# Kernel tuning notes

Hardware: AMD Instinct MI355X
Metric: run time of the kernel (lower is better)

Reference implementation:

```python
import jax, jax.numpy as jnp
import numpy as np

N_NODES = 50000
N_EDGES = 400000
N_E2E = 1600000
F_N = 128
F_E = 64
H = 128
NEG_SLOPE = 0.2


def setup_inputs() -> dict:
    key = jax.random.key(0)
    ks = jax.random.split(key, 8)
    x_node = jax.random.normal(ks[0], (N_NODES, F_N), dtype=jnp.float32)
    edge_attr = jax.random.normal(ks[1], (N_EDGES, F_E), dtype=jnp.float32)
    edge_index = jax.random.randint(ks[2], (2, N_EDGES), 0, N_NODES, dtype=jnp.int64)
    edge_edge_index = jax.random.randint(ks[3], (2, N_E2E), 0, N_EDGES, dtype=jnp.int64)
    # xavier-uniform-like init scales
    def xavier(k, shape):
        fan_in, fan_out = shape[1], shape[0]
        lim = jnp.sqrt(6.0 / (fan_in + fan_out)).astype(jnp.float32)
        return jax.random.uniform(k, shape, jnp.float32, -lim, lim)
    Wn = xavier(ks[4], (H, F_N))          # lin_node.weight
    We = xavier(ks[5], (H, F_E))          # lin_edge.weight
    an = xavier(ks[6], (1, 2 * H))[0]     # att_n.weight, flattened to [2H]
    ae = xavier(ks[7], (1, 2 * H))[0]     # att_e.weight, flattened to [2H]
    return {"x_node": x_node, "edge_attr": edge_attr, "edge_index": edge_index,
            "edge_edge_index": edge_edge_index, "Wn": Wn, "We": We, "an": an, "ae": ae}


def _segment_softmax(score, seg, num_segments):
    m = jax.ops.segment_max(score, seg, num_segments=num_segments)
    ex = jnp.exp(score - m[seg])
    denom = jax.ops.segment_sum(ex, seg, num_segments=num_segments)
    return ex / denom[seg]


def reference(x_node, edge_attr, edge_index, edge_edge_index, Wn, We, an, ae):
    E = edge_attr.shape[0]
    h = x_node @ Wn.T      # [N, H]
    g = edge_attr @ We.T   # [E, H]

    # ---- node-based neighbors of each edge (its 2 endpoints) ----
    u, v = edge_index[0], edge_index[1]
    e_rep = jnp.concatenate([jnp.arange(E), jnp.arange(E)])   # segment ids [2E]
    n_for_e = jnp.concatenate([u, v])                          # [2E]
    a1, a2 = an[:H], an[H:]   # split cat([g, h]) @ an into two dots
    h_nbr = h[n_for_e]                                         # [2E, H]
    score_ne = jax.nn.leaky_relu(g[e_rep] @ a1 + h_nbr @ a2, NEG_SLOPE)
    alpha_ne = _segment_softmax(score_ne, e_rep, E)
    s_n = jax.ops.segment_sum(alpha_ne[:, None] * h_nbr, e_rep, num_segments=E)
    cnt_n = jax.ops.segment_sum(jnp.ones_like(alpha_ne), e_rep, num_segments=E)
    e_from_nodes = jax.nn.relu(s_n / jnp.maximum(cnt_n, 1.0)[:, None])

    # ---- edge-based neighbors (edges sharing a node) ----
    e_src, e_nbr = edge_edge_index[0], edge_edge_index[1]
    b1, b2 = ae[:H], ae[H:]
    g_nbr = g[e_nbr]                                           # [E2E, H]
    score_ee = jax.nn.leaky_relu(g[e_src] @ b1 + g_nbr @ b2, NEG_SLOPE)
    alpha_ee = _segment_softmax(score_ee, e_src, E)
    s_e = jax.ops.segment_sum(alpha_ee[:, None] * g_nbr, e_src, num_segments=E)
    cnt_e = jax.ops.segment_sum(jnp.ones_like(alpha_ee), e_src, num_segments=E)
    e_from_edges = jax.nn.relu(s_e / jnp.maximum(cnt_e, 1.0)[:, None])

    return jnp.concatenate([e_from_nodes, e_from_edges], axis=-1)  # [E, 2H]
```

## Files before the change

kernel.cpp:

```cpp
#include <hip/hip_runtime.h>
#include <hip/hip_bf16.h>

#define N_NODES 50000
#define N_EDGES 400000
#define N_E2E   1600000
#define F_N 128
#define F_E 64
#define H   128
#define NEG_SLOPE 0.2f
#define CAP 24

typedef __hip_bfloat16 bf16;
typedef __attribute__((ext_vector_type(8))) short bf16x8;
typedef __attribute__((ext_vector_type(4))) float f32x4;


__device__ inline float2 upk(unsigned int v) {
    union { unsigned int u; float f; } a, b;
    a.u = v << 16;
    b.u = v & 0xffff0000u;
    return make_float2(a.f, b.f);
}
__device__ inline unsigned int f2bfbits(float f) {
    union { float f; unsigned int u; } a; a.f = f;
    return (a.u + 0x7fffu + ((a.u >> 16) & 1u)) >> 16;
}
__device__ inline float lrelu(float x) { return x > 0.f ? x : NEG_SLOPE * x; }

__device__ inline float ldf(const void* p, size_t i, int isf32) {
    return isf32 ? ((const float*)p)[i] : __bfloat162float(((const bf16*)p)[i]);
}
__device__ inline int ldidx(const int* p, long long k, int is64) {
    return is64 ? p[2 * k] : p[k];
}

__device__ inline void loadA4(const void* p, int isf32, size_t idx, float* v) {
    if (isf32) {
        const float4 f = *(const float4*)((const float*)p + idx);
        v[0] = f.x; v[1] = f.y; v[2] = f.z; v[3] = f.w;
    } else {
        const uint2 u = *(const uint2*)((const bf16*)p + idx);
        float2 a = upk(u.x), b = upk(u.y);
        v[0] = a.x; v[1] = a.y; v[2] = b.x; v[3] = b.y;
    }
}
__device__ inline void stash(unsigned short* s, unsigned off, unsigned loOff, const float* v) {
    unsigned hb[4], lb[4];
    #pragma unroll
    for (int j = 0; j < 4; ++j) {
        unsigned hbits = f2bfbits(v[j]);
        union { unsigned u; float f; } hf; hf.u = hbits << 16;
        hb[j] = hbits;
        lb[j] = f2bfbits(v[j] - hf.f);
    }
    *(uint2*)((char*)s + off)         = make_uint2(hb[0] | (hb[1] << 16), hb[2] | (hb[3] << 16));
    *(uint2*)((char*)s + loOff + off) = make_uint2(lb[0] | (lb[1] << 16), lb[2] | (lb[3] << 16));
}

__global__ __launch_bounds__(256) void k_pat(unsigned int* __restrict__ o,
                                             long long n, unsigned int pat) {
    long long i = (long long)blockIdx.x * 256 + threadIdx.x;
    long long stride = (long long)gridDim.x * 256;
    for (; i < n; i += stride) o[i] = pat;
}

__global__ __launch_bounds__(256) void k_init(const unsigned int* x, const unsigned int* ea,
                                              const unsigned int* Wn, const unsigned int* We,
                                              const unsigned int* an, const unsigned int* ae,
                                              const unsigned int* ei, const unsigned int* eei,
                                              int* __restrict__ flags, int* __restrict__ cnt) {
    int i = blockIdx.x * 256 + threadIdx.x;
    if (i < N_EDGES) cnt[i] = 0;
    if (blockIdx.x == 0) {
        int t = threadIdx.x;
        if (t < 6) {
            const unsigned int* p = t == 0 ? x : t == 1 ? ea : t == 2 ? Wn
                                  : t == 3 ? We : t == 4 ? an : ae;
            int inrange = 0;
            for (int k = 0; k < 64; k++) {
                unsigned int e = (p[k] >> 7) & 0xFFu;
                if (e >= 100u && e <= 140u) inrange++;
            }
            flags[t] = (inrange < 48) ? 1 : 0;
        } else if (t < 8) {
            const unsigned int* p = (t == 6) ? ei : eei;
            int allzero = 1;
            for (int k = 1; k < 128; k += 2) if (p[k] != 0u) allzero = 0;
            flags[t] = allzero;
        }
    }
}

template<int K>
__global__ __launch_bounds__(256) void k_gemm(const void* __restrict__ A,
                                              const void* __restrict__ W,
                                              const int* __restrict__ flags,
                                              int faIdx, int fwIdx, int M,
                                              bf16* __restrict__ out,
                                              const void* __restrict__ an,
                                              const void* __restrict__ ae,
                                              float* __restrict__ dot0,
                                              float* __restrict__ dot1,
                                              float* __restrict__ dot2) {
    __shared__ unsigned short sA[2 * 128 * 64];
    __shared__ unsigned short sB[2 * 128 * 64];
    constexpr unsigned ALO = 128u * 64u * 2u;
    constexpr unsigned BLO = 128u * 64u * 2u;
    const int t = threadIdx.x;
    const int e0 = blockIdx.x * 128;
    const int fa = flags[faIdx], fw = flags[fwIdx];
    const int w = t >> 6, l = t & 63;
    const int lr = l & 15, lk = l >> 4;
    const unsigned sxor = (unsigned)((l & 7) << 4);

    f32x4 acc[8][2];
    #pragma unroll
    for (int mt = 0; mt < 8; ++mt)
        #pragma unroll
        for (int nt = 0; nt < 2; ++nt)
            acc[mt][nt] = (f32x4){0.f, 0.f, 0.f, 0.f};

    #pragma unroll
    for (int kt = 0; kt < K / 64; ++kt) {
        if (kt) __syncthreads();
        #pragma unroll
        for (int c0 = 0; c0 < 2048; c0 += 256) {
            int c = c0 + t;
            int r = c >> 4, kc = (c & 15) << 2;
            float v[4];
            int e = e0 + r;
            if (e < M) loadA4(A, fa, (size_t)e * K + kt * 64 + kc, v);
            else { v[0] = v[1] = v[2] = v[3] = 0.f; }
            stash(sA, (unsigned)((r * 64 + kc) * 2) ^ ((unsigned)(r & 7) << 4), ALO, v);
        }
        #pragma unroll
        for (int c0 = 0; c0 < 2048; c0 += 256) {
            int c = c0 + t;
            int r = c >> 4, kc = (c & 15) << 2;
            float v[4];
            loadA4(W, fw, (size_t)r * K + kt * 64 + kc, v);
            stash(sB, (unsigned)((r * 64 + kc) * 2) ^ ((unsigned)(r & 7) << 4), BLO, v);
        }
        __syncthreads();
        const char* pA = (const char*)sA;
        const char* pB = (const char*)sB;
        #pragma unroll
        for (int ks = 0; ks < 2; ++ks) {
            const unsigned ko = (unsigned)((ks * 32 + lk * 8) * 2);
            bf16x8 bh[2], bl[2];
            #pragma unroll
            for (int nt = 0; nt < 2; ++nt) {
                unsigned off = ((unsigned)((w * 32 + nt * 16 + lr) * 128) + ko) ^ sxor;
                bh[nt] = *(const bf16x8*)(pB + off);
                bl[nt] = *(const bf16x8*)(pB + BLO + off);
            }
            #pragma unroll
            for (int mt = 0; mt < 8; ++mt) {
                unsigned off = ((unsigned)((mt * 16 + lr) * 128) + ko) ^ sxor;
                bf16x8 ah = *(const bf16x8*)(pA + off);
                bf16x8 al = *(const bf16x8*)(pA + ALO + off);
                #pragma unroll
                for (int nt = 0; nt < 2; ++nt) {
                    acc[mt][nt] = __builtin_amdgcn_mfma_f32_16x16x32_bf16(ah, bh[nt], acc[mt][nt], 0, 0, 0);
                    acc[mt][nt] = __builtin_amdgcn_mfma_f32_16x16x32_bf16(ah, bl[nt], acc[mt][nt], 0, 0, 0);
                    acc[mt][nt] = __builtin_amdgcn_mfma_f32_16x16x32_bf16(al, bh[nt], acc[mt][nt], 0, 0, 0);
                }
            }
        }
    }
    #pragma unroll
    for (int mt = 0; mt < 8; ++mt)
        #pragma unroll
        for (int i = 0; i < 4; ++i) {
            int e = e0 + mt * 16 + lk * 4 + i;
            if (e < M) {
                #pragma unroll
                for (int nt = 0; nt < 2; ++nt)
                    out[(size_t)e * 128 + (w * 32 + nt * 16 + lr)] =
                        __float2bfloat16(acc[mt][nt][i]);
            }
        }
    __syncthreads();
    float* sd = (float*)sA;
    const int fan = flags[4], fae = flags[5];
    const int c0i = w * 32 + lr, c1i = c0i + 16;
    constexpr int ND = (K == 64) ? 3 : 1;
    float av[ND][2];
    if constexpr (K == 64) {
        av[0][0] = ldf(an, c0i, fan);      av[0][1] = ldf(an, c1i, fan);
        av[1][0] = ldf(ae, c0i, fae);      av[1][1] = ldf(ae, c1i, fae);
        av[2][0] = ldf(ae, H + c0i, fae);  av[2][1] = ldf(ae, H + c1i, fae);
    } else {
        av[0][0] = ldf(an, H + c0i, fan);  av[0][1] = ldf(an, H + c1i, fan);
    }
    #pragma unroll
    for (int d = 0; d < ND; ++d)
        #pragma unroll
        for (int mt = 0; mt < 8; ++mt)
            #pragma unroll
            for (int i = 0; i < 4; ++i) {
                float p = acc[mt][0][i] * av[d][0] + acc[mt][1][i] * av[d][1];
                #pragma unroll
                for (int off = 1; off < 16; off <<= 1) p += __shfl_xor(p, off, 64);
                if (lr == 0) sd[(d * 4 + w) * 128 + mt * 16 + lk * 4 + i] = p;
            }
    __syncthreads();
    for (int idx = t; idx < 128 * ND; idx += 256) {
        int d = idx >> 7, row = idx & 127;
        float vs = sd[(d * 4 + 0) * 128 + row] + sd[(d * 4 + 1) * 128 + row]
                 + sd[(d * 4 + 2) * 128 + row] + sd[(d * 4 + 3) * 128 + row];
        int e = e0 + row;
        if (e < M) (d == 0 ? dot0 : d == 1 ? dot1 : dot2)[e] = vs;
    }
}

__global__ __launch_bounds__(256) void k_node(const int* __restrict__ ei,
                                              const int* __restrict__ flags,
                                              const bf16* __restrict__ h,
                                              const float* __restrict__ ha2,
                                              const float* __restrict__ ga1,
                                              void* __restrict__ out) {
    int e = blockIdx.x * 8 + (threadIdx.x >> 5);
    int lane = threadIdx.x & 31;
    int is64 = flags[6], fo = flags[0];
    int u = ldidx(ei, e, is64);
    int v = ldidx(ei, (long long)N_EDGES + e, is64);
    float ga = ga1[e];
    float su = lrelu(ga + ha2[u]);
    float sv = lrelu(ga + ha2[v]);
    float m = fmaxf(su, sv);
    float eu = __expf(su - m), ev = __expf(sv - m);
    float inv = 1.f / (eu + ev);
    float wu = (eu * inv) * 0.5f;
    float wv = (ev * inv) * 0.5f;
    const uint2* hw = (const uint2*)h;
    uint2 qu = hw[(size_t)u * 32 + lane];
    uint2 qv = hw[(size_t)v * 32 + lane];
    float2 u0 = upk(qu.x), u1 = upk(qu.y);
    float2 v0 = upk(qv.x), v1 = upk(qv.y);
    float c0 = wu * u0.x + wv * v0.x;
    float c1 = wu * u0.y + wv * v0.y;
    float c2 = wu * u1.x + wv * v1.x;
    float c3 = wu * u1.y + wv * v1.y;
    float r0 = c0 > 0.f ? c0 : 0.f; if (c0 != c0) r0 = c0;
    float r1 = c1 > 0.f ? c1 : 0.f; if (c1 != c1) r1 = c1;
    float r2 = c2 > 0.f ? c2 : 0.f; if (c2 != c2) r2 = c2;
    float r3 = c3 > 0.f ? c3 : 0.f; if (c3 != c3) r3 = c3;
    if (fo) {
        float4* o = (float4*)((float*)out + (size_t)e * 256 + 4 * lane);
        *o = make_float4(r0, r1, r2, r3);
    } else {
        uint2 pk;
        pk.x = f2bfbits(r0) | (f2bfbits(r1) << 16);
        pk.y = f2bfbits(r2) | (f2bfbits(r3) << 16);
        ((uint2*)((bf16*)out + (size_t)e * 256))[lane] = pk;
    }
}

__global__ __launch_bounds__(256) void k_fill(const int* __restrict__ eei,
                                              const int* __restrict__ flags,
                                              int* __restrict__ cnt,
                                              int* __restrict__ bucket) {
    int k = blockIdx.x * 256 + threadIdx.x;
    if (k >= N_E2E) return;
    int is64 = flags[7];
    int src = ldidx(eei, k, is64);
    int nbr = ldidx(eei, (long long)N_E2E + k, is64);
    int j = atomicAdd(&cnt[src], 1);
    if (j < CAP) bucket[(size_t)src * CAP + j] = nbr;
}

__global__ __launch_bounds__(256) void k_ee(const int* __restrict__ cnt,
                                            const int* __restrict__ bucket,
                                            const float* __restrict__ gb1,
                                            const float* __restrict__ gb2,
                                            const bf16* __restrict__ g,
                                            const int* __restrict__ flags,
                                            void* __restrict__ out) {
    int e = blockIdx.x * 8 + (threadIdx.x >> 5);
    int lane = threadIdx.x & 31;
    int base = threadIdx.x & 32;
    int fo = flags[0];
    int c = cnt[e]; if (c > CAP) c = CAP;
    float s = -1e30f; int mynbr = 0;
    if (lane < c) {
        mynbr = bucket[(size_t)e * CAP + lane];
        s = lrelu(gb1[e] + gb2[mynbr]);
    }
    float m = s;
    #pragma unroll
    for (int off = 16; off; off >>= 1) m = fmaxf(m, __shfl_xor(m, off, 64));
    float ex = (lane < c) ? __expf(s - m) : 0.f;
    float denom = ex;
    #pragma unroll
    for (int off = 16; off; off >>= 1) denom += __shfl_xor(denom, off, 64);
    float invd = denom > 0.f ? 1.f / denom : 0.f;
    float ax = 0.f, ay = 0.f, az = 0.f, aw = 0.f;
    const uint2* __restrict__ gw = (const uint2*)g;
    for (int j0 = 0; j0 < c; j0 += 4) {
        float a0 = __shfl(ex, base + j0, 64) * invd;
        float a1 = __shfl(ex, base + j0 + 1, 64) * invd;
        float a2 = __shfl(ex, base + j0 + 2, 64) * invd;
        float a3 = __shfl(ex, base + j0 + 3, 64) * invd;
        int n0 = __shfl(mynbr, base + j0, 64);
        int n1 = __shfl(mynbr, base + j0 + 1, 64);
        int n2 = __shfl(mynbr, base + j0 + 2, 64);
        int n3 = __shfl(mynbr, base + j0 + 3, 64);
        uint2 q0 = gw[(size_t)n0 * 32 + lane];
        uint2 q1 = gw[(size_t)n1 * 32 + lane];
        uint2 q2 = gw[(size_t)n2 * 32 + lane];
        uint2 q3 = gw[(size_t)n3 * 32 + lane];
        float2 l0 = upk(q0.x), h0 = upk(q0.y);
        float2 l1 = upk(q1.x), h1 = upk(q1.y);
        float2 l2 = upk(q2.x), h2 = upk(q2.y);
        float2 l3 = upk(q3.x), h3 = upk(q3.y);
        ax += a0 * l0.x; ay += a0 * l0.y; az += a0 * h0.x; aw += a0 * h0.y;
        ax += a1 * l1.x; ay += a1 * l1.y; az += a1 * h1.x; aw += a1 * h1.y;
        ax += a2 * l2.x; ay += a2 * l2.y; az += a2 * h2.x; aw += a2 * h2.y;
        ax += a3 * l3.x; ay += a3 * l3.y; az += a3 * h3.x; aw += a3 * h3.y;
    }
    float invc = 1.f / (float)(c > 0 ? c : 1);
    ax *= invc; ay *= invc; az *= invc; aw *= invc;
    float r0 = ax > 0.f ? ax : 0.f; if (ax != ax) r0 = ax;
    float r1 = ay > 0.f ? ay : 0.f; if (ay != ay) r1 = ay;
    float r2 = az > 0.f ? az : 0.f; if (az != az) r2 = az;
    float r3 = aw > 0.f ? aw : 0.f; if (aw != aw) r3 = aw;
    if (fo) {
        float4* o = (float4*)((float*)out + (size_t)e * 256 + H + 4 * lane);
        *o = make_float4(r0, r1, r2, r3);
    } else {
        uint2 pk;
        pk.x = f2bfbits(r0) | (f2bfbits(r1) << 16);
        pk.y = f2bfbits(r2) | (f2bfbits(r3) << 16);
        ((uint2*)((bf16*)out + (size_t)e * 256 + H))[lane] = pk;
    }
}

extern "C" void kernel_launch(void* const* d_in, const int* in_sizes, int n_in,
                              void* d_out, int out_size, void* d_ws, size_t ws_size,
                              hipStream_t stream) {
    (void)out_size;
    unsigned int* outw = (unsigned int*)d_out;
    const long long OUTW = (long long)N_EDGES * 256 / 2;

    const int* s = in_sizes;
    auto isEI  = [](int v) { return v == 2 * N_EDGES || v == 4 * N_EDGES; };
    auto isEEI = [](int v) { return v == 2 * N_E2E || v == 4 * N_E2E; };
    bool okA = n_in == 8 && s[0] == N_NODES * F_N && s[1] == N_EDGES * F_E &&
               isEI(s[2]) && isEEI(s[3]) && s[4] == H * F_N && s[5] == H * F_E &&
               s[6] == 2 * H && s[7] == 2 * H;
    bool okB = n_in == 8 && s[0] == H * F_E && s[1] == H * F_N && s[2] == 2 * H &&
               s[3] == 2 * H && s[4] == N_EDGES * F_E && isEEI(s[5]) && isEI(s[6]) &&
               s[7] == N_NODES * F_N;
    if (!okA && !okB) {
        k_pat<<<2048, 256, 0, stream>>>(outw, OUTW, 0x44804480u);
        return;
    }
    const void *x, *ea, *Wn, *We, *an, *ae; const int *ei, *eei;
    if (okA) {
        x = d_in[0]; ea = d_in[1]; ei = (const int*)d_in[2]; eei = (const int*)d_in[3];
        Wn = d_in[4]; We = d_in[5]; an = d_in[6]; ae = d_in[7];
    } else {
        We = d_in[0]; Wn = d_in[1]; ae = d_in[2]; an = d_in[3];
        ea = d_in[4]; eei = (const int*)d_in[5]; ei = (const int*)d_in[6]; x = d_in[7];
    }

    char* w0 = (char*)d_ws; char* w = w0;
    auto alloc = [&](size_t bytes) -> char* {
        char* p = w; w += (bytes + 255) & ~(size_t)255; return p;
    };
    int*   flags  = (int*)alloc(256);
    float* ha2    = (float*)alloc((size_t)N_NODES * 4);
    float* ga1    = (float*)alloc((size_t)N_EDGES * 4);
    float* gb1    = (float*)alloc((size_t)N_EDGES * 4);
    float* gb2    = (float*)alloc((size_t)N_EDGES * 4);
    int*   cnt    = (int*)alloc((size_t)N_EDGES * 4);
    int*   bucket = (int*)alloc((size_t)N_EDGES * CAP * 4);
    bf16*  h      = (bf16*)alloc((size_t)N_NODES * H * 2);
    bf16*  g      = (bf16*)alloc((size_t)N_EDGES * H * 2);
    if ((size_t)(w - w0) > ws_size) {
        k_pat<<<2048, 256, 0, stream>>>(outw, OUTW, 0x44004400u);
        return;
    }


    k_init<<<(N_EDGES + 255) / 256, 256, 0, stream>>>((const unsigned int*)x,
            (const unsigned int*)ea, (const unsigned int*)Wn, (const unsigned int*)We,
            (const unsigned int*)an, (const unsigned int*)ae,
            (const unsigned int*)ei, (const unsigned int*)eei, flags, cnt);
    k_gemm<128><<<(N_NODES + 127) / 128, 256, 0, stream>>>(x, Wn, flags, 0, 2, N_NODES,
                                                           h, an, ae, ha2, nullptr, nullptr);
    k_gemm<64><<<N_EDGES / 128, 256, 0, stream>>>(ea, We, flags, 1, 3, N_EDGES,
                                                  g, an, ae, ga1, gb1, gb2);
    k_fill<<<(N_E2E + 255) / 256, 256, 0, stream>>>(eei, flags, cnt, bucket);
    k_node<<<N_EDGES / 8, 256, 0, stream>>>(ei, flags, h, ha2, ga1, d_out);
    k_ee<<<N_EDGES / 8, 256, 0, stream>>>(cnt, bucket, gb1, gb2, g, flags, d_out);
}
```

Baseline: 996.5 us.

## Pre-split weights into bf16 planes, vectorize bucket fill, fuse node and edge attention kernels

Adds a small kernel that converts Wn and We once into bf16 hi/lo planes. The GEMM now reads B fragments straight from global memory, which removes the per-block weight staging into LDS and the conversion work. The bucket fill kernel now handles two edge-edge entries per thread with vector loads. The node-attention and edge-attention kernels are merged into one, which drops a launch and lets the output row be written in one pass. The trade-off is uncoalesced global loads of weights inside the MFMA loop (likely cache hits) and higher register pressure in the fused kernel.

```diff
diff --git a/kernel.cpp b/kernel.cpp
--- a/kernel.cpp
+++ b/kernel.cpp
@@ -91,11 +91,36 @@
     }
 }
 
+__global__ __launch_bounds__(256) void k_planes(const void* __restrict__ Wn,
+                                                const void* __restrict__ We,
+                                                const int* __restrict__ flags,
+                                                unsigned short* __restrict__ wnhi,
+                                                unsigned short* __restrict__ wnlo,
+                                                unsigned short* __restrict__ wehi,
+                                                unsigned short* __restrict__ welo) {
+    int i = blockIdx.x * 256 + threadIdx.x;
+    if (i < 128 * 64) {
+        float v = ldf(We, i, flags[3]);
+        unsigned hb = f2bfbits(v);
+        union { unsigned u; float f; } hf; hf.u = hb << 16;
+        wehi[i] = (unsigned short)hb;
+        welo[i] = (unsigned short)f2bfbits(v - hf.f);
+    } else if (i < 128 * 64 + 128 * 128) {
+        int j = i - 128 * 64;
+        float v = ldf(Wn, j, flags[2]);
+        unsigned hb = f2bfbits(v);
+        union { unsigned u; float f; } hf; hf.u = hb << 16;
+        wnhi[j] = (unsigned short)hb;
+        wnlo[j] = (unsigned short)f2bfbits(v - hf.f);
+    }
+}
+
 template<int K>
 __global__ __launch_bounds__(256) void k_gemm(const void* __restrict__ A,
-                                              const void* __restrict__ W,
                                               const int* __restrict__ flags,
-                                              int faIdx, int fwIdx, int M,
+                                              int faIdx, int M,
+                                              const unsigned short* __restrict__ whi,
+                                              const unsigned short* __restrict__ wlo,
                                               bf16* __restrict__ out,
                                               const void* __restrict__ an,
                                               const void* __restrict__ ae,
@@ -103,12 +128,10 @@
                                               float* __restrict__ dot1,
                                               float* __restrict__ dot2) {
     __shared__ unsigned short sA[2 * 128 * 64];
-    __shared__ unsigned short sB[2 * 128 * 64];
     constexpr unsigned ALO = 128u * 64u * 2u;
-    constexpr unsigned BLO = 128u * 64u * 2u;
     const int t = threadIdx.x;
     const int e0 = blockIdx.x * 128;
-    const int fa = flags[faIdx], fw = flags[fwIdx];
+    const int fa = flags[faIdx];
     const int w = t >> 6, l = t & 63;
     const int lr = l & 15, lk = l >> 4;
     const unsigned sxor = (unsigned)((l & 7) << 4);
@@ -133,26 +156,17 @@
             else { v[0] = v[1] = v[2] = v[3] = 0.f; }
             stash(sA, (unsigned)((r * 64 + kc) * 2) ^ ((unsigned)(r & 7) << 4), ALO, v);
         }
-        #pragma unroll
-        for (int c0 = 0; c0 < 2048; c0 += 256) {
-            int c = c0 + t;
-            int r = c >> 4, kc = (c & 15) << 2;
-            float v[4];
-            loadA4(W, fw, (size_t)r * K + kt * 64 + kc, v);
-            stash(sB, (unsigned)((r * 64 + kc) * 2) ^ ((unsigned)(r & 7) << 4), BLO, v);
-        }
         __syncthreads();
         const char* pA = (const char*)sA;
-        const char* pB = (const char*)sB;
         #pragma unroll
         for (int ks = 0; ks < 2; ++ks) {
             const unsigned ko = (unsigned)((ks * 32 + lk * 8) * 2);
             bf16x8 bh[2], bl[2];
             #pragma unroll
             for (int nt = 0; nt < 2; ++nt) {
-                unsigned off = ((unsigned)((w * 32 + nt * 16 + lr) * 128) + ko) ^ sxor;
-                bh[nt] = *(const bf16x8*)(pB + off);
-                bl[nt] = *(const bf16x8*)(pB + BLO + off);
+                size_t boff = (size_t)(w * 32 + nt * 16 + lr) * K + kt * 64 + ks * 32 + lk * 8;
+                bh[nt] = *(const bf16x8*)(whi + boff);
+                bl[nt] = *(const bf16x8*)(wlo + boff);
             }
             #pragma unroll
             for (int mt = 0; mt < 8; ++mt) {
@@ -214,22 +228,59 @@
     }
 }
 
-__global__ __launch_bounds__(256) void k_node(const int* __restrict__ ei,
+__global__ __launch_bounds__(256) void k_fill(const int* __restrict__ eei,
                                               const int* __restrict__ flags,
-                                              const bf16* __restrict__ h,
-                                              const float* __restrict__ ha2,
-                                              const float* __restrict__ ga1,
-                                              void* __restrict__ out) {
+                                              int* __restrict__ cnt,
+                                              int* __restrict__ bucket) {
+    int k2 = blockIdx.x * 256 + threadIdx.x;
+    if (k2 * 2 >= N_E2E) return;
+    int is64 = flags[7];
+    int s0, s1, n0, n1;
+    if (is64) {
+        uint4 qs = ((const uint4*)eei)[k2];
+        uint4 qn = ((const uint4*)(eei + 2 * (size_t)N_E2E))[k2];
+        s0 = (int)qs.x; s1 = (int)qs.z;
+        n0 = (int)qn.x; n1 = (int)qn.z;
+    } else {
+        uint2 qs = ((const uint2*)eei)[k2];
+        uint2 qn = ((const uint2*)(eei + (size_t)N_E2E))[k2];
+        s0 = (int)qs.x; s1 = (int)qs.y;
+        n0 = (int)qn.x; n1 = (int)qn.y;
+    }
+    int j0 = atomicAdd(&cnt[s0], 1); if (j0 < CAP) bucket[(size_t)s0 * CAP + j0] = n0;
+    int j1 = atomicAdd(&cnt[s1], 1); if (j1 < CAP) bucket[(size_t)s1 * CAP + j1] = n1;
+}
+
+__global__ __launch_bounds__(256) void k_att(const int* __restrict__ ei,
+                                             const int* __restrict__ flags,
+                                             const bf16* __restrict__ h,
+                                             const float* __restrict__ ha2,
+                                             const float* __restrict__ ga1,
+                                             const int* __restrict__ cnt,
+                                             const int* __restrict__ bucket,
+                                             const float* __restrict__ gb1,
+                                             const float* __restrict__ gb2,
+                                             const bf16* __restrict__ g,
+                                             void* __restrict__ out) {
     int e = blockIdx.x * 8 + (threadIdx.x >> 5);
     int lane = threadIdx.x & 31;
+    int base = threadIdx.x & 32;
     int is64 = flags[6], fo = flags[0];
+
+    int c = cnt[e]; if (c > CAP) c = CAP;
     int u = ldidx(ei, e, is64);
     int v = ldidx(ei, (long long)N_EDGES + e, is64);
+    float s = -1e30f; int mynbr = 0;
+    if (lane < c) {
+        mynbr = bucket[(size_t)e * CAP + lane];
+        s = lrelu(gb1[e] + gb2[mynbr]);
+    }
+
     float ga = ga1[e];
     float su = lrelu(ga + ha2[u]);
     float sv = lrelu(ga + ha2[v]);
-    float m = fmaxf(su, sv);
-    float eu = __expf(su - m), ev = __expf(sv - m);
+    float mn = fmaxf(su, sv);
+    float eu = __expf(su - mn), ev = __expf(sv - mn);
     float inv = 1.f / (eu + ev);
     float wu = (eu * inv) * 0.5f;
     float wv = (ev * inv) * 0.5f;
@@ -242,51 +293,11 @@
     float c1 = wu * u0.y + wv * v0.y;
     float c2 = wu * u1.x + wv * v1.x;
     float c3 = wu * u1.y + wv * v1.y;
-    float r0 = c0 > 0.f ? c0 : 0.f; if (c0 != c0) r0 = c0;
-    float r1 = c1 > 0.f ? c1 : 0.f; if (c1 != c1) r1 = c1;
-    float r2 = c2 > 0.f ? c2 : 0.f; if (c2 != c2) r2 = c2;
-    float r3 = c3 > 0.f ? c3 : 0.f; if (c3 != c3) r3 = c3;
-    if (fo) {
-        float4* o = (float4*)((float*)out + (size_t)e * 256 + 4 * lane);
-        *o = make_float4(r0, r1, r2, r3);
-    } else {
-        uint2 pk;
-        pk.x = f2bfbits(r0) | (f2bfbits(r1) << 16);
-        pk.y = f2bfbits(r2) | (f2bfbits(r3) << 16);
-        ((uint2*)((bf16*)out + (size_t)e * 256))[lane] = pk;
-    }
-}
-
-__global__ __launch_bounds__(256) void k_fill(const int* __restrict__ eei,
-                                              const int* __restrict__ flags,
-                                              int* __restrict__ cnt,
-                                              int* __restrict__ bucket) {
-    int k = blockIdx.x * 256 + threadIdx.x;
-    if (k >= N_E2E) return;
-    int is64 = flags[7];
-    int src = ldidx(eei, k, is64);
-    int nbr = ldidx(eei, (long long)N_E2E + k, is64);
-    int j = atomicAdd(&cnt[src], 1);
-    if (j < CAP) bucket[(size_t)src * CAP + j] = nbr;
-}
-
-__global__ __launch_bounds__(256) void k_ee(const int* __restrict__ cnt,
-                                            const int* __restrict__ bucket,
-                                            const float* __restrict__ gb1,
-                                            const float* __restrict__ gb2,
-                                            const bf16* __restrict__ g,
-                                            const int* __restrict__ flags,
-                                            void* __restrict__ out) {
-    int e = blockIdx.x * 8 + (threadIdx.x >> 5);
-    int lane = threadIdx.x & 31;
-    int base = threadIdx.x & 32;
-    int fo = flags[0];
-    int c = cnt[e]; if (c > CAP) c = CAP;
-    float s = -1e30f; int mynbr = 0;
-    if (lane < c) {
-        mynbr = bucket[(size_t)e * CAP + lane];
-        s = lrelu(gb1[e] + gb2[mynbr]);
-    }
+    float nr0 = c0 > 0.f ? c0 : 0.f; if (c0 != c0) nr0 = c0;
+    float nr1 = c1 > 0.f ? c1 : 0.f; if (c1 != c1) nr1 = c1;
+    float nr2 = c2 > 0.f ? c2 : 0.f; if (c2 != c2) nr2 = c2;
+    float nr3 = c3 > 0.f ? c3 : 0.f; if (c3 != c3) nr3 = c3;
+
     float m = s;
     #pragma unroll
     for (int off = 16; off; off >>= 1) m = fmaxf(m, __shfl_xor(m, off, 64));
@@ -321,18 +332,24 @@
     }
     float invc = 1.f / (float)(c > 0 ? c : 1);
     ax *= invc; ay *= invc; az *= invc; aw *= invc;
-    float r0 = ax > 0.f ? ax : 0.f; if (ax != ax) r0 = ax;
-    float r1 = ay > 0.f ? ay : 0.f; if (ay != ay) r1 = ay;
-    float r2 = az > 0.f ? az : 0.f; if (az != az) r2 = az;
-    float r3 = aw > 0.f ? aw : 0.f; if (aw != aw) r3 = aw;
+    float er0 = ax > 0.f ? ax : 0.f; if (ax != ax) er0 = ax;
+    float er1 = ay > 0.f ? ay : 0.f; if (ay != ay) er1 = ay;
+    float er2 = az > 0.f ? az : 0.f; if (az != az) er2 = az;
+    float er3 = aw > 0.f ? aw : 0.f; if (aw != aw) er3 = aw;
+
     if (fo) {
-        float4* o = (float4*)((float*)out + (size_t)e * 256 + H + 4 * lane);
-        *o = make_float4(r0, r1, r2, r3);
+        float4* o0 = (float4*)((float*)out + (size_t)e * 256 + 4 * lane);
+        *o0 = make_float4(nr0, nr1, nr2, nr3);
+        float4* o1 = (float4*)((float*)out + (size_t)e * 256 + H + 4 * lane);
+        *o1 = make_float4(er0, er1, er2, er3);
     } else {
-        uint2 pk;
-        pk.x = f2bfbits(r0) | (f2bfbits(r1) << 16);
-        pk.y = f2bfbits(r2) | (f2bfbits(r3) << 16);
-        ((uint2*)((bf16*)out + (size_t)e * 256 + H))[lane] = pk;
+        uint2 pk0, pk1;
+        pk0.x = f2bfbits(nr0) | (f2bfbits(nr1) << 16);
+        pk0.y = f2bfbits(nr2) | (f2bfbits(nr3) << 16);
+        pk1.x = f2bfbits(er0) | (f2bfbits(er1) << 16);
+        pk1.y = f2bfbits(er2) | (f2bfbits(er3) << 16);
+        ((uint2*)((bf16*)out + (size_t)e * 256))[lane] = pk0;
+        ((uint2*)((bf16*)out + (size_t)e * 256 + H))[lane] = pk1;
     }
 }
 
@@ -378,6 +395,10 @@
     int*   bucket = (int*)alloc((size_t)N_EDGES * CAP * 4);
     bf16*  h      = (bf16*)alloc((size_t)N_NODES * H * 2);
     bf16*  g      = (bf16*)alloc((size_t)N_EDGES * H * 2);
+    unsigned short* wnhi = (unsigned short*)alloc(128 * 128 * 2);
+    unsigned short* wnlo = (unsigned short*)alloc(128 * 128 * 2);
+    unsigned short* wehi = (unsigned short*)alloc(128 * 64 * 2);
+    unsigned short* welo = (unsigned short*)alloc(128 * 64 * 2);
     if ((size_t)(w - w0) > ws_size) {
         k_pat<<<2048, 256, 0, stream>>>(outw, OUTW, 0x44004400u);
         return;
@@ -388,11 +409,12 @@
             (const unsigned int*)ea, (const unsigned int*)Wn, (const unsigned int*)We,
             (const unsigned int*)an, (const unsigned int*)ae,
             (const unsigned int*)ei, (const unsigned int*)eei, flags, cnt);
-    k_gemm<128><<<(N_NODES + 127) / 128, 256, 0, stream>>>(x, Wn, flags, 0, 2, N_NODES,
-                                                           h, an, ae, ha2, nullptr, nullptr);
-    k_gemm<64><<<N_EDGES / 128, 256, 0, stream>>>(ea, We, flags, 1, 3, N_EDGES,
-                                                  g, an, ae, ga1, gb1, gb2);
-    k_fill<<<(N_E2E + 255) / 256, 256, 0, stream>>>(eei, flags, cnt, bucket);
-    k_node<<<N_EDGES / 8, 256, 0, stream>>>(ei, flags, h, ha2, ga1, d_out);
-    k_ee<<<N_EDGES / 8, 256, 0, stream>>>(cnt, bucket, gb1, gb2, g, flags, d_out);
-}
+    k_planes<<<96, 256, 0, stream>>>(Wn, We, flags, wnhi, wnlo, wehi, welo);
+    k_gemm<128><<<(N_NODES + 127) / 128, 256, 0, stream>>>(x, flags, 0, N_NODES,
+            wnhi, wnlo, h, an, ae, ha2, nullptr, nullptr);
+    k_gemm<64><<<N_EDGES / 128, 256, 0, stream>>>(ea, flags, 1, N_EDGES,
+            wehi, welo, g, an, ae, ga1, gb1, gb2);
+    k_fill<<<(N_E2E / 2 + 255) / 256, 256, 0, stream>>>(eei, flags, cnt, bucket);
+    k_att<<<N_EDGES / 8, 256, 0, stream>>>(ei, flags, h, ha2, ga1,
+                                           cnt, bucket, gb1, gb2, g, d_out);
+}
```

New measurement: 938.1 us. 1.06x faster.
